# Performance work log

Hardware: AMD Instinct MI355X
Metric: run time of the kernel (lower is better)

The kernel has to match this reference:

```python
import jax, jax.numpy as jnp
import numpy as np

jax.config.update("jax_enable_x64", True)

MANT_SCALE = 8388608.0  # 2**23


def _decode_fp32_bits(bits):
    """[..., 32] {0,1} pulses (MSB-first IEEE-754 float32) -> float64 value."""
    f64 = jnp.float64
    sign = 1.0 - 2.0 * bits[..., 0].astype(f64)
    e = jnp.einsum('...j,j->...', bits[..., 1:9].astype(f64),
                   jnp.exp2(jnp.arange(7, -1, -1, dtype=f64)))
    frac = jnp.einsum('...j,j->...', bits[..., 9:32].astype(f64),
                      jnp.exp2(-jnp.arange(1, 24, dtype=f64)))
    normal = sign * jnp.exp2(e - 127.0) * (1.0 + frac)
    subnorm = sign * jnp.exp2(-126.0) * frac
    return jnp.where(e > 0, normal, subnorm)


def _encode_fp32_bits(y):
    """float64 value already on the fp32 grid -> [..., 32] {0,1} pulses (MSB-first)."""
    f64 = jnp.float64
    sbit = (y < 0).astype(f64)
    a = jnp.abs(y)
    e = jnp.clip(jnp.floor(jnp.log2(jnp.where(a > 0, a, 1.0))), -126.0, 127.0)
    eb = jnp.where(a > 0, e + 127.0, 0.0)          # biased exponent, 0 for zero/subnormal
    frac = jnp.where(eb > 0, a * jnp.exp2(-e) - 1.0, a * jnp.exp2(126.0))
    mant = frac * MANT_SCALE                        # exact integer for fp32-grid y
    ebits = jnp.mod(jnp.floor(eb[..., None] * jnp.exp2(-jnp.arange(7, -1, -1, dtype=f64))), 2.0)
    mbits = jnp.mod(jnp.floor(mant[..., None] * jnp.exp2(-jnp.arange(22, -1, -1, dtype=f64))), 2.0)
    bits = jnp.concatenate([sbit[..., None], ebits, mbits], axis=-1)
    return jnp.where((a > 0)[..., None], bits, 0.0).astype(jnp.float32)


def setup_inputs() -> dict:
    rng = np.random.default_rng(0)
    vals = (rng.standard_normal((1, 2048, 1024)) * 2.0).astype(np.float32)
    words = vals.view(np.uint32)
    shifts = np.arange(31, -1, -1, dtype=np.uint32)
    bits = ((words[..., None] >> shifts) & np.uint32(1)).astype(np.float32)
    return {"x": jnp.asarray(bits)}


def reference(x):
    # GELU(x) ~= x * sigmoid(1.702 * x), all intermediates in fp64 (as the
    # gate-level pipeline does), final result rounded once to fp32 bits.
    xv = _decode_fp32_bits(x)
    y64 = xv * jax.nn.sigmoid(1.702 * xv)
    y32 = y64.astype(jnp.float32).astype(jnp.float64)  # FP64 -> FP32 rounding
    return _encode_fp32_bits(y32)
```

## Files before the change

### kernel.cpp

```cpp
#include <hip/hip_runtime.h>
#include <math.h>


#define LN2C 0x1.62e42fefa39efp-1

typedef unsigned int u32x4 __attribute__((ext_vector_type(4)));

__device__ __forceinline__ uint32_t nib_transpose8(uint32_t x, int p) {
  uint32_t r;
  r = __shfl_xor(x, 1);
  x = (p & 1) ? ((x & 0xF0F0F0F0u) | ((r >> 4) & 0x0F0F0F0Fu))
              : ((x & 0x0F0F0F0Fu) | ((r << 4) & 0xF0F0F0F0u));
  r = __shfl_xor(x, 2);
  x = (p & 2) ? ((x & 0xFF00FF00u) | ((r >> 8) & 0x00FF00FFu))
              : ((x & 0x00FF00FFu) | ((r << 8) & 0xFF00FF00u));
  r = __shfl_xor(x, 4);
  x = (p & 4) ? ((x & 0xFFFF0000u) | ((r >> 16) & 0x0000FFFFu))
              : ((x & 0x0000FFFFu) | ((r << 16) & 0xFFFF0000u));
  return x;
}

__device__ __forceinline__ uint32_t nib_reverse(uint32_t x) {
  uint32_t b = __builtin_bswap32(x);
  return ((b >> 4) & 0x0F0F0F0Fu) | ((b << 4) & 0xF0F0F0F0u);
}

__global__ __launch_bounds__(256) void spike_gelu_kernel(
    const u32x4* __restrict__ in, u32x4* __restrict__ out,
    int n_vals, int n_tiles) {
#pragma clang fp contract(off)
  const double LN2 = LN2C;
  __shared__ double Wdec[8];
  __shared__ double Lms[23];
  __shared__ double E1t[256];
  __shared__ double Vdec[23];
  __shared__ double P2t[254];
  __shared__ uint32_t etab[256];
  __shared__ u32x4 lut16[16];

  const int tid = threadIdx.x;
  const int lane = tid & 63;
  const int kp = lane & 7;
  const int wid = tid >> 6;
  const int n_chunks = n_vals * 8;
  const int tstep = gridDim.x;

  int tile = blockIdx.x;

  u32x4 A[8];
  {
    const int cb = tile * 2048 + wid * 512 + lane;
#pragma unroll
    for (int i = 0; i < 8; ++i) {
      int g = cb + i * 64;
      u32x4 b = {0u, 0u, 0u, 0u};
      if (g < n_chunks) b = __builtin_nontemporal_load(&in[g]);
      A[i] = b;
    }
  }

  if (tid < 8) Wdec[tid] = exp((double)(7 - tid) * LN2);
  if (tid >= 31 && tid < 54) Lms[tid - 31] = exp((double)(31 - tid) * LN2);
  __syncthreads();
  if (tid == 0) {
    E1t[0] = exp(-126.0 * LN2);
  } else {
    double e_c = 0.0;
#pragma unroll
    for (int j = 0; j < 8; ++j)
      if ((tid >> (7 - j)) & 1) e_c = e_c + Wdec[j];
    E1t[tid] = exp((e_c - 127.0) * LN2);
  }
  if (tid < 23) Vdec[tid] = exp((double)(-1 - tid) * LN2);
  if (tid < 254) P2t[tid] = exp((double)(126 - tid) * LN2);
  if (tid < 16) {
    u32x4 e;
    e.x = ((tid >> 3) & 1u) * 0x3F800000u;
    e.y = ((tid >> 2) & 1u) * 0x3F800000u;
    e.z = ((tid >> 1) & 1u) * 0x3F800000u;
    e.w = (tid & 1u) * 0x3F800000u;
    lut16[tid] = e;
  }
  if (tid >= 1 && tid < 255) {
    double eb = (double)tid;
    uint32_t r = 0;
#pragma unroll
    for (int sc = 7; sc >= 0; --sc) {
      double f = floor(eb * Lms[sc]);
      double md = f - 2.0 * floor(0.5 * f);
      r |= ((uint32_t)md) << (23 + sc);
    }
    etab[tid] = r;
  } else if (tid == 255 || tid == 0) {
    etab[tid] = 0u;
  }
  __syncthreads();

  for (;;) {
    uint32_t X = 0u;
#pragma unroll
    for (int i = 0; i < 8; ++i) {
      u32x4 b = A[i];
      uint32_t nib = (((b.x >> 23) & 1u) << 3) | (((b.y >> 23) & 1u) << 2) |
                     (((b.z >> 23) & 1u) << 1) | ((b.w >> 23) & 1u);
      X |= nib << (4 * i);
    }
    __builtin_amdgcn_sched_barrier(0);

    const int ntile = tile + tstep;
    const bool havenext = ntile < n_tiles;
    if (havenext) {
      const int cb = ntile * 2048 + wid * 512 + lane;
#pragma unroll
      for (int i = 0; i < 8; ++i) {
        int g = cb + i * 64;
        u32x4 b = {0u, 0u, 0u, 0u};
        if (g < n_chunks) b = __builtin_nontemporal_load(&in[g]);
        A[i] = b;
      }
    }

    uint32_t w0 = nib_reverse(nib_transpose8(X, kp));

    const int vwave = tile * 256 + wid * 64;
    const int v0 = vwave + kp * 8 + (lane >> 3);
    const bool ok0 = v0 < n_vals;

    double f0 = 0.0;
#pragma unroll
    for (int j = 0; j < 23; ++j)
      if ((w0 >> (22 - j)) & 1u) f0 = f0 + Vdec[j];
    uint32_t ei0 = (w0 >> 23) & 0xFFu;
    double sg0 = (w0 >> 31) ? -1.0 : 1.0;
    double fa0 = ei0 ? (1.0 + f0) : f0;
    double x0 = (sg0 * E1t[ei0]) * fa0;

    double t0 = 1.702 * x0;
    double e0v = exp(-t0);
    double s0 = 1.0 / (1.0 + e0v);
    double y0 = x0 * s0;
    float yf0 = (float)y0;
    double yd0 = (double)yf0;

    double a0 = fabs(yd0);
    uint32_t yb0 = __float_as_uint(yf0);
    uint32_t Ef0 = (yb0 >> 23) & 0xFFu;
    uint32_t mbf0 = yb0 & 0x7FFFFFu;
    int e00 = (Ef0 == 0u) ? -126 : (int)Ef0 - 127;
    bool pw0 = ok0 && (a0 > 0.0) && (Ef0 != 0u) && (mbf0 == 0u);
    if (__builtin_expect(pw0, 0)) {
      double e0 = floor(log(a0) / LN2);
      e00 = (int)fmin(fmax(e0, -126.0), 127.0);
    }
    double p20 = P2t[e00 + 126];
    double m10 = a0 * p20;
    double mant0 = (m10 - 1.0) * 8388608.0;
    int M0 = (int)rint(mant0);
    uint32_t mb0 = ((uint32_t)M0) & 0x7FFFFFu;
    int T0 = M0 ? __builtin_ctz((uint32_t)M0) : 23;
    int L0 = T0 < 22 ? T0 : 22;
    for (int sc = 0; sc <= L0; ++sc) {
      double f = floor(mant0 * Lms[sc]);
      mb0 = (mb0 & ~(1u << sc)) | (((uint32_t)(((int)f) & 1)) << sc);
    }
    uint32_t ob0 = (yb0 & 0x80000000u) | etab[e00 + 127] | mb0;
    ob0 = (ok0 && a0 > 0.0) ? ob0 : 0u;

    uint32_t Z = nib_transpose8(nib_reverse(ob0), kp);
    const int cb = tile * 2048 + wid * 512 + lane;
#pragma unroll
    for (int i = 0; i < 8; ++i) {
      int g = cb + i * 64;
      if (g < n_chunks) {
        u32x4 o = lut16[(Z >> (4 * i)) & 0xFu];
        __builtin_nontemporal_store(o, &out[g]);
      }
    }

    if (!havenext) break;
    tile = ntile;
  }
}

extern "C" void kernel_launch(void* const* d_in, const int* in_sizes, int n_in,
                              void* d_out, int out_size, void* d_ws, size_t ws_size,
                              hipStream_t stream) {
  int n_vals = in_sizes[0] / 32;
  int n_tiles = (n_vals + 255) / 256;
  int grid = n_tiles < 1024 ? n_tiles : 1024;
  spike_gelu_kernel<<<grid, 256, 0, stream>>>(
      (const u32x4*)d_in[0], (u32x4*)d_out, n_vals, n_tiles);
}
```

Measured before the change: 419.3 us.

## Double-buffer input tiles two iterations ahead and set occupancy launch bound

Prefetch now runs two tiles ahead using two register buffers (A and Bb) alternating in an unrolled-by-two loop, so more global loads are in flight while the GELU chain and stores run. The launch bounds also request 4 waves per SIMD to limit register growth. The second buffer adds 32 VGPRs, which may force spills or lower occupancy. This is a memory-bound kernel (8 MB in, 8 MB out, grid of 1024 blocks covering 8192 tiles), so the deeper prefetch is aimed at load latency.

```diff
diff --git a/kernel.cpp b/kernel.cpp
--- a/kernel.cpp
+++ b/kernel.cpp
@@ -25,7 +25,31 @@
   return ((b >> 4) & 0x0F0F0F0Fu) | ((b << 4) & 0xF0F0F0F0u);
 }
 
-__global__ __launch_bounds__(256) void spike_gelu_kernel(
+__device__ __forceinline__ void load_tile(const u32x4* __restrict__ in,
+                                          int cb, int n_chunks,
+                                          u32x4 (&B)[8]) {
+#pragma unroll
+  for (int i = 0; i < 8; ++i) {
+    int g = cb + i * 64;
+    u32x4 b = {0u, 0u, 0u, 0u};
+    if (g < n_chunks) b = __builtin_nontemporal_load(&in[g]);
+    B[i] = b;
+  }
+}
+
+__device__ __forceinline__ uint32_t pack_tile(const u32x4 (&B)[8], int kp) {
+  uint32_t X = 0u;
+#pragma unroll
+  for (int i = 0; i < 8; ++i) {
+    u32x4 b = B[i];
+    uint32_t nib = (((b.x >> 23) & 1u) << 3) | (((b.y >> 23) & 1u) << 2) |
+                   (((b.z >> 23) & 1u) << 1) | ((b.w >> 23) & 1u);
+    X |= nib << (4 * i);
+  }
+  return nib_reverse(nib_transpose8(X, kp));
+}
+
+__global__ __launch_bounds__(256, 4) void spike_gelu_kernel(
     const u32x4* __restrict__ in, u32x4* __restrict__ out,
     int n_vals, int n_tiles) {
 #pragma clang fp contract(off)
@@ -44,20 +68,12 @@
   const int wid = tid >> 6;
   const int n_chunks = n_vals * 8;
   const int tstep = gridDim.x;
+  const int laneoff = wid * 512 + lane;
 
   int tile = blockIdx.x;
 
-  u32x4 A[8];
-  {
-    const int cb = tile * 2048 + wid * 512 + lane;
-#pragma unroll
-    for (int i = 0; i < 8; ++i) {
-      int g = cb + i * 64;
-      u32x4 b = {0u, 0u, 0u, 0u};
-      if (g < n_chunks) b = __builtin_nontemporal_load(&in[g]);
-      A[i] = b;
-    }
-  }
+  u32x4 A[8], Bb[8];
+  load_tile(in, tile * 2048 + laneoff, n_chunks, A);
 
   if (tid < 8) Wdec[tid] = exp((double)(7 - tid) * LN2);
   if (tid >= 31 && tid < 54) Lms[tid - 31] = exp((double)(31 - tid) * LN2);
@@ -96,33 +112,11 @@
   }
   __syncthreads();
 
-  for (;;) {
-    uint32_t X = 0u;
-#pragma unroll
-    for (int i = 0; i < 8; ++i) {
-      u32x4 b = A[i];
-      uint32_t nib = (((b.x >> 23) & 1u) << 3) | (((b.y >> 23) & 1u) << 2) |
-                     (((b.z >> 23) & 1u) << 1) | ((b.w >> 23) & 1u);
-      X |= nib << (4 * i);
-    }
-    __builtin_amdgcn_sched_barrier(0);
-
-    const int ntile = tile + tstep;
-    const bool havenext = ntile < n_tiles;
-    if (havenext) {
-      const int cb = ntile * 2048 + wid * 512 + lane;
-#pragma unroll
-      for (int i = 0; i < 8; ++i) {
-        int g = cb + i * 64;
-        u32x4 b = {0u, 0u, 0u, 0u};
-        if (g < n_chunks) b = __builtin_nontemporal_load(&in[g]);
-        A[i] = b;
-      }
-    }
-
-    uint32_t w0 = nib_reverse(nib_transpose8(X, kp));
-
-    const int vwave = tile * 256 + wid * 64;
+  if (tile + tstep < n_tiles)
+    load_tile(in, (tile + tstep) * 2048 + laneoff, n_chunks, Bb);
+
+  auto chain_store = [&](uint32_t w0, int t) {
+    const int vwave = t * 256 + wid * 64;
     const int v0 = vwave + kp * 8 + (lane >> 3);
     const bool ok0 = v0 < n_vals;
 
@@ -167,7 +161,7 @@
     ob0 = (ok0 && a0 > 0.0) ? ob0 : 0u;
 
     uint32_t Z = nib_transpose8(nib_reverse(ob0), kp);
-    const int cb = tile * 2048 + wid * 512 + lane;
+    const int cb = t * 2048 + laneoff;
 #pragma unroll
     for (int i = 0; i < 8; ++i) {
       int g = cb + i * 64;
@@ -176,9 +170,28 @@
         __builtin_nontemporal_store(o, &out[g]);
       }
     }
-
-    if (!havenext) break;
-    tile = ntile;
+  };
+
+  for (;;) {
+    {
+      uint32_t w0 = pack_tile(A, kp);
+      __builtin_amdgcn_sched_barrier(0);
+      int t2 = tile + 2 * tstep;
+      if (t2 < n_tiles) load_tile(in, t2 * 2048 + laneoff, n_chunks, A);
+      chain_store(w0, tile);
+    }
+    if (tile + tstep >= n_tiles) break;
+
+    {
+      int tb = tile + tstep;
+      uint32_t w0 = pack_tile(Bb, kp);
+      __builtin_amdgcn_sched_barrier(0);
+      int t3 = tb + 2 * tstep;
+      if (t3 < n_tiles) load_tile(in, t3 * 2048 + laneoff, n_chunks, Bb);
+      chain_store(w0, tb);
+    }
+    tile += 2 * tstep;
+    if (tile >= n_tiles) break;
   }
 }
 
```

Result: no change. 416.6 us (median of 2 runs) (-0.6%).
